# Performance work log

Measured on AMD Instinct MI355X. Metric: run time of the kernel, lower is better.

Reference implementation:

```python
import jax, jax.numpy as jnp
import numpy as np

N_NODES = 100000
N_EDGES = 1600000
D_FEAT = 128
UNITS = 128
LEAKY_ALPHA = 0.2  # tf.nn.leaky_relu default


def setup_inputs() -> dict:
    key = jax.random.key(0)
    k1, k2, k3, k4 = jax.random.split(key, 4)
    node_states = jax.random.normal(k1, (N_NODES, D_FEAT), dtype=jnp.float32)
    edges = jax.random.randint(k2, (N_EDGES, 2), 0, N_NODES, dtype=jnp.int64)
    kernel = jax.random.normal(k3, (D_FEAT, UNITS), dtype=jnp.float32) * (1.0 / np.sqrt(D_FEAT))
    kernel_attention = jax.random.normal(k4, (2 * UNITS, 1), dtype=jnp.float32) * (1.0 / np.sqrt(2 * UNITS))
    return {
        "node_states": node_states,
        "edges": edges,
        "kernel": kernel,
        "kernel_attention": kernel_attention,
    }


def reference(node_states, edges, kernel, kernel_attention):
    n = node_states.shape[0]
    tgt_idx = edges[:, 0]
    src_idx = edges[:, 1]

    # node_states_transformed: [N, units]
    h = node_states @ kernel

    # Attention logits. concat([tgt, src]) @ ka == tgt @ ka_t + src @ ka_s
    # (avoids materializing the [E, 2*units] concat).
    ka_t = kernel_attention[:UNITS, 0]   # [units]
    ka_s = kernel_attention[UNITS:, 0]   # [units]
    score_t = h @ ka_t                   # [N]
    score_s = h @ ka_s                   # [N]
    e = score_t[tgt_idx] + score_s[src_idx]              # [E]
    e = jax.nn.leaky_relu(e, negative_slope=LEAKY_ALPHA)
    e = jnp.exp(jnp.clip(e, -2.0, 2.0))

    # Segment softmax over incoming edges of each target node.
    sum_e = jax.ops.segment_sum(e, tgt_idx, num_segments=n)  # [N]
    attention = e / (sum_e[tgt_idx] + 1e-9)                  # [E]

    # Weighted scatter-sum of source messages.
    messages = h[src_idx] * attention[:, None]               # [E, units]
    output = jax.ops.segment_sum(messages, tgt_idx, num_segments=n)  # [N, units]
    return output
```

## Files before the change

kernel.cpp:

```cpp
#include <hip/hip_runtime.h>
#include <stdint.h>

typedef unsigned short ushort_t;
typedef __attribute__((ext_vector_type(8))) short short8;
typedef __attribute__((ext_vector_type(4))) float float4v;
typedef __attribute__((ext_vector_type(2))) float float2v;

#define N_NODES 100000
#define N_EDGES 1600000
#define D 128
#define NB_GEMM 1563
#define NBP     782
#define NB_B1   250
#define EPB     6400
#define BUCKETS 782
#define CAP     2560

static __device__ __forceinline__ float2v up2(uint32_t u) {
    float2v r;
    r.x = __builtin_bit_cast(float, u << 16);
    r.y = __builtin_bit_cast(float, u & 0xffff0000u);
    return r;
}
static __device__ __forceinline__ ushort_t f2bf(float f) {
    uint32_t u = __builtin_bit_cast(uint32_t, f);
    uint32_t r = u + 0x7fffu + ((u >> 16) & 1u);
    return (ushort_t)(r >> 16);
}
static __device__ __forceinline__ float edge_e(float s) {
    float x = (s >= 0.0f) ? s : 0.2f * s;
    x = fminf(fmaxf(x, -2.0f), 2.0f);
    return __expf(x);
}

__global__ void __launch_bounds__(256) prep_kernel(const float* __restrict__ W,
                                                   const float* __restrict__ KA,
                                                   float* __restrict__ wa,
                                                   ushort_t* __restrict__ WT,
                                                   const int* __restrict__ E,
                                                   int* __restrict__ eflag) {
    __shared__ int s;
    int b = blockIdx.x, t = threadIdx.x;
    int i = b * 256 + t;
    if (b < 64) {
        int k = i >> 7, nn = i & 127;
        int kb = k >> 5, q = (k >> 3) & 3, j = k & 7;
        int tt = nn >> 4, l = nn & 15;
        WT[((kb * 8 + tt) * 64 + q * 16 + l) * 8 + j] = f2bf(W[i]);
    } else if (b == 64) {
        if (t == 0) s = 0;
        __syncthreads();
        int nz = 0;
#pragma unroll
        for (int j = 0; j < 8; j++)
            if (E[(t + j * 256) * 2 + 1] != 0) nz = 1;
        if (nz) atomicOr(&s, 1);
        __syncthreads();
        if (t == 0) *eflag = (s == 0) ? 1 : 0;
    } else if (b == 65) {
        int half = t >> 7, k = t & 127;
        const float* kav = KA + half * 128;
        const float* wrow = W + k * 128;
        float acc = 0.0f;
#pragma unroll 8
        for (int j = 0; j < 128; j++) acc += wrow[j] * kav[j];
        wa[half * 128 + k] = acc;
    }
}

__global__ void __launch_bounds__(256) mega1_kernel(const float* __restrict__ X,
                                                    const ushort_t* __restrict__ WT,
                                                    const float* __restrict__ wa,
                                                    ushort_t* __restrict__ H,
                                                    float* __restrict__ st,
                                                    float* __restrict__ ss,
                                                    int M,
                                                    const int* __restrict__ E,
                                                    const int* __restrict__ eflag,
                                                    int* __restrict__ sortedE,
                                                    ushort_t* __restrict__ bmat,
                                                    ushort_t* __restrict__ lofs) {
    __shared__ ushort_t ob[4][16 * 136];
    if (blockIdx.x >= NBP) {
        int eb = blockIdx.x - NBP;
        int t = threadIdx.x;
        int* lhist = (int*)ob;
        int* lpart = ((int*)ob) + 1024;
        for (int j = t; j < 1024; j += 256) lhist[j] = 0;
        __syncthreads();
        int i64 = *eflag;
        int base = eb * EPB;
        for (int j = 0; j < 25; j++) {
            int i = base + j * 256 + t;
            int tgt = i64 ? E[i * 4] : E[i * 2];
            if ((unsigned)tgt >= (unsigned)N_NODES) tgt = 0;
            atomicAdd(&lhist[tgt >> 7], 1);
        }
        __syncthreads();
        int c0 = lhist[t * 4], c1 = lhist[t * 4 + 1];
        int c2 = lhist[t * 4 + 2], c3 = lhist[t * 4 + 3];
        int sum = c0 + c1 + c2 + c3;
        lpart[t] = sum;
        __syncthreads();
        for (int off = 1; off < 256; off <<= 1) {
            int x = (t >= off) ? lpart[t - off] : 0;
            __syncthreads();
            lpart[t] += x;
            __syncthreads();
        }
        int e0 = lpart[t] - sum;
        int e1 = e0 + c0, e2 = e1 + c1, e3 = e2 + c2;
        int cc[4] = {c0, c1, c2, c3};
        int ee[4] = {e0, e1, e2, e3};
#pragma unroll
        for (int k = 0; k < 4; k++) {
            int bb = t * 4 + k;
            if (bb < BUCKETS) {
                bmat[eb * BUCKETS + bb] = (ushort_t)cc[k];
                lofs[eb * BUCKETS + bb] = (ushort_t)ee[k];
            }
        }
        lhist[t * 4] = e0; lhist[t * 4 + 1] = e1;
        lhist[t * 4 + 2] = e2; lhist[t * 4 + 3] = e3;
        __syncthreads();
        for (int j = 0; j < 25; j++) {
            int i = base + j * 256 + t;
            int tgt, src;
            if (i64) { tgt = E[i * 4]; src = E[i * 4 + 2]; }
            else     { tgt = E[i * 2]; src = E[i * 2 + 1]; }
            if ((unsigned)tgt >= (unsigned)N_NODES) tgt = 0;
            if ((unsigned)src >= (unsigned)N_NODES) src = 0;
            int pos = atomicAdd(&lhist[tgt >> 7], 1);
            if (pos < EPB) sortedE[base + pos] = ((tgt & 127) << 17) | src;
        }
        return;
    }
    int tid = threadIdx.x;
    int wave = tid >> 6, lane = tid & 63;
    int quad = lane >> 4, l16 = lane & 15;
    ushort_t* obw = ob[wave];
    const short8* Bf = (const short8*)WT;

    int t0 = blockIdx.x;
    int nt = (t0 + NBP < NB_GEMM) ? 2 : 1;

    float4 f[8];
    {
        int ar = t0 * 64 + wave * 16 + l16; if (ar >= M) ar = M - 1;
        const float* xr = X + (size_t)ar * D + quad * 8;
#pragma unroll
        for (int kb = 0; kb < 4; kb++) {
            f[kb * 2]     = *(const float4*)(xr + kb * 32);
            f[kb * 2 + 1] = *(const float4*)(xr + kb * 32 + 4);
        }
    }
    for (int it = 0; it < nt; it++) {
        int m0 = (t0 + it * NBP) * 64 + wave * 16;
        float4 nf[8];
        if (it + 1 < nt) {
            int ar = (t0 + NBP) * 64 + wave * 16 + l16; if (ar >= M) ar = M - 1;
            const float* xr = X + (size_t)ar * D + quad * 8;
#pragma unroll
            for (int kb = 0; kb < 4; kb++) {
                nf[kb * 2]     = *(const float4*)(xr + kb * 32);
                nf[kb * 2 + 1] = *(const float4*)(xr + kb * 32 + 4);
            }
        }
        short8 a[4];
        float sct = 0.0f, scs = 0.0f;
#pragma unroll
        for (int kb = 0; kb < 4; kb++) {
            float4 f0 = f[kb * 2], f1 = f[kb * 2 + 1];
            const float* wt0 = wa + kb * 32 + quad * 8;
            float4 t0v = *(const float4*)(wt0);
            float4 t1v = *(const float4*)(wt0 + 4);
            float4 s0v = *(const float4*)(wt0 + 128);
            float4 s1v = *(const float4*)(wt0 + 132);
            sct += f0.x * t0v.x + f0.y * t0v.y + f0.z * t0v.z + f0.w * t0v.w
                 + f1.x * t1v.x + f1.y * t1v.y + f1.z * t1v.z + f1.w * t1v.w;
            scs += f0.x * s0v.x + f0.y * s0v.y + f0.z * s0v.z + f0.w * s0v.w
                 + f1.x * s1v.x + f1.y * s1v.y + f1.z * s1v.z + f1.w * s1v.w;
            short8 v;
            v[0] = (short)f2bf(f0.x); v[1] = (short)f2bf(f0.y);
            v[2] = (short)f2bf(f0.z); v[3] = (short)f2bf(f0.w);
            v[4] = (short)f2bf(f1.x); v[5] = (short)f2bf(f1.y);
            v[6] = (short)f2bf(f1.z); v[7] = (short)f2bf(f1.w);
            a[kb] = v;
        }
        sct += __shfl_xor(sct, 16); sct += __shfl_xor(sct, 32);
        scs += __shfl_xor(scs, 16); scs += __shfl_xor(scs, 32);
        if (quad == 0 && m0 + l16 < M) { st[m0 + l16] = sct; ss[m0 + l16] = scs; }

        float4v acc[8] = {};
#pragma unroll
        for (int kb = 0; kb < 4; kb++) {
#pragma unroll
            for (int t = 0; t < 8; t++) {
                short8 b = Bf[(kb * 8 + t) * 64 + lane];
                acc[t] = __builtin_amdgcn_mfma_f32_16x16x32_bf16(a[kb], b, acc[t], 0, 0, 0);
            }
        }
#pragma unroll
        for (int t = 0; t < 8; t++)
#pragma unroll
            for (int r = 0; r < 4; r++)
                obw[(quad * 4 + r) * 136 + t * 16 + l16] = f2bf(acc[t][r]);
#pragma unroll
        for (int p = 0; p < 4; p++) {
            int row = p * 4 + quad;
            int orow = m0 + row;
            if (orow < M) {
                uint4 v = *(const uint4*)(&obw[row * 136 + l16 * 8]);
                *(uint4*)(H + (size_t)orow * D + l16 * 8) = v;
            }
        }
        if (it + 1 < nt) {
#pragma unroll
            for (int j = 0; j < 8; j++) f[j] = nf[j];
        }
    }
}

__global__ void __launch_bounds__(512) agg2_kernel(const ushort_t* __restrict__ bmat,
                                                   const ushort_t* __restrict__ lofs,
                                                   const int* __restrict__ sortedE,
                                                   const float* __restrict__ st,
                                                   const float* __restrict__ ss,
                                                   const ushort_t* __restrict__ H,
                                                   float* __restrict__ out) {
    __shared__ int stage[CAP];
    __shared__ int sortedLoc[CAP];
    __shared__ int lpart[512];
    __shared__ int lh[128];
    __shared__ int lrp[129];
    int b = blockIdx.x, t = threadIdx.x;
    int cnt = 0, sst = 0;
    if (t < NB_B1) {
        cnt = bmat[t * BUCKETS + b];
        sst = lofs[t * BUCKETS + b];
    }
    lpart[t] = cnt;
    __syncthreads();
    for (int off = 1; off < 512; off <<= 1) {
        int x = (t >= off) ? lpart[t - off] : 0;
        __syncthreads();
        lpart[t] += x;
        __syncthreads();
    }
    int soff  = lpart[t] - cnt;
    int total = lpart[511];
    if (total > CAP) total = CAP;
    if (t < 128) lh[t] = 0;
    for (int k = 0; k < cnt; k++) {
        int idx = soff + k;
        if (idx < CAP) stage[idx] = sortedE[t * EPB + sst + k];
    }
    __syncthreads();
    for (int j = t; j < total; j += 512)
        atomicAdd(&lh[stage[j] >> 17], 1);
    __syncthreads();
    int v = (t < 128) ? lh[t] : 0;
    if (t < 128) lpart[t] = v;
    __syncthreads();
    for (int off = 1; off < 128; off <<= 1) {
        int x = (t >= off && t < 128) ? lpart[t - off] : 0;
        __syncthreads();
        if (t < 128) lpart[t] += x;
        __syncthreads();
    }
    if (t < 128) {
        int ex = lpart[t] - v;
        lrp[t] = ex;
        lh[t]  = ex;
    }
    if (t == 0) lrp[128] = total;
    __syncthreads();
    for (int j = t; j < total; j += 512) {
        int p = stage[j];
        int pos = atomicAdd(&lh[p >> 17], 1);
        if (pos < total) sortedLoc[pos] = p & 0x1FFFF;
    }
    __syncthreads();
    int wave = t >> 6, lane = t & 63;
    int g = lane >> 4, l = lane & 15;
    for (int nd = wave; nd < 128; nd += 8) {
        int gnode = b * 128 + nd;
        if (gnode >= N_NODES) break;
        int start = lrp[nd], end = lrp[nd + 1];
        float stn = st[gnode];
        float den = 0.0f;
        float2v acc2[4] = {};
        int m = start + g;
        for (; m + 4 < end; m += 8) {
            int s0 = sortedLoc[m], s1 = sortedLoc[m + 4];
            float e0 = edge_e(stn + ss[s0]);
            float e1 = edge_e(stn + ss[s1]);
            den += e0 + e1;
            uint4 p0 = *(const uint4*)(H + ((unsigned)s0 << 7) + l * 8);
            uint4 p1 = *(const uint4*)(H + ((unsigned)s1 << 7) + l * 8);
            float2v E0 = {e0, e0}, E1 = {e1, e1};
            acc2[0] += E0 * up2(p0.x) + E1 * up2(p1.x);
            acc2[1] += E0 * up2(p0.y) + E1 * up2(p1.y);
            acc2[2] += E0 * up2(p0.z) + E1 * up2(p1.z);
            acc2[3] += E0 * up2(p0.w) + E1 * up2(p1.w);
        }
        if (m < end) {
            int s0 = sortedLoc[m];
            float e0 = edge_e(stn + ss[s0]);
            den += e0;
            uint4 p0 = *(const uint4*)(H + ((unsigned)s0 << 7) + l * 8);
            float2v E0 = {e0, e0};
            acc2[0] += E0 * up2(p0.x);
            acc2[1] += E0 * up2(p0.y);
            acc2[2] += E0 * up2(p0.z);
            acc2[3] += E0 * up2(p0.w);
        }
        den += __shfl_xor(den, 16);
        den += __shfl_xor(den, 32);
        float r[8];
#pragma unroll
        for (int j = 0; j < 4; j++) {
            float a0 = acc2[j].x, a1 = acc2[j].y;
            a0 += __shfl_xor(a0, 16); a0 += __shfl_xor(a0, 32);
            a1 += __shfl_xor(a1, 16); a1 += __shfl_xor(a1, 32);
            r[j * 2] = a0; r[j * 2 + 1] = a1;
        }
        float inv = 1.0f / (den + 1e-9f);
        if (g == 0) {
            float4 o0 = make_float4(r[0] * inv, r[1] * inv, r[2] * inv, r[3] * inv);
            float4 o1 = make_float4(r[4] * inv, r[5] * inv, r[6] * inv, r[7] * inv);
            *(float4*)(out + (size_t)gnode * D + l * 8) = o0;
            *(float4*)(out + (size_t)gnode * D + l * 8 + 4) = o1;
        }
    }
}

extern "C" void kernel_launch(void* const* d_in, const int* in_sizes, int n_in,
                              void* d_out, int out_size, void* d_ws, size_t ws_size,
                              hipStream_t stream) {
    const float* X  = (const float*)d_in[0];
    const int*   E  = (const int*)d_in[1];
    const float* W  = (const float*)d_in[2];
    const float* KA = (const float*)d_in[3];
    for (int i = 0; i < n_in; i++) {
        int s = in_sizes[i];
        if (s == N_NODES * D)      X  = (const float*)d_in[i];
        else if (s == N_EDGES * 2) E  = (const int*)d_in[i];
        else if (s == D * D)       W  = (const float*)d_in[i];
        else if (s == 2 * D)       KA = (const float*)d_in[i];
    }
    float* out = (float*)d_out;

    char* ws = (char*)d_ws;
    ushort_t* H        = (ushort_t*)(ws + 0);
    float*    wa       = (float*)   (ws + 25600000);
    float*    st       = (float*)   (ws + 25601024);
    float*    ssb      = (float*)   (ws + 26001024);
    int*      sortedE  = (int*)     (ws + 26401024);
    ushort_t* bmat     = (ushort_t*)(ws + 32801024);
    ushort_t* lofs     = (ushort_t*)(ws + 33192032);
    int*      eflag    = (int*)     (ws + 33583040);
    ushort_t* WT       = (ushort_t*)(ws + 33583072);

    prep_kernel<<<66, 256, 0, stream>>>(W, KA, wa, WT, E, eflag);
    mega1_kernel<<<NBP + NB_B1, 256, 0, stream>>>(X, WT, wa, H, st, ssb,
                                                  N_NODES, E, eflag,
                                                  sortedE, bmat, lofs);
    agg2_kernel<<<BUCKETS, 512, 0, stream>>>(bmat, lofs, sortedE, st, ssb,
                                             H, out);
}
```

Before: 229.9 us.

## Store H in permuted column order to drop LDS transpose; shuffle-based scans

The GEMM epilogue now packs each lane's MFMA accumulators straight into bf16 and writes them to H in a permuted column order, removing the LDS staging buffer and its transpose. The aggregation kernel undoes the permutation by writing each lane's eight outputs at stride 16, which replaces two float4 stores with eight scalar stores. The block-level prefix sums in the aggregation kernel switch from barrier-heavy LDS Hillis-Steele loops to wave shuffles plus a small per-wave sum array, which cuts the number of __syncthreads. This trades LDS traffic and barriers for less vectorized output stores.

```diff
diff --git a/kernel.cpp b/kernel.cpp
--- a/kernel.cpp
+++ b/kernel.cpp
@@ -22,10 +22,15 @@
     r.y = __builtin_bit_cast(float, u & 0xffff0000u);
     return r;
 }
+static __device__ __forceinline__ uint32_t f2bf_u(float f) {
+    uint32_t u = __builtin_bit_cast(uint32_t, f);
+    return (u + 0x7fffu + ((u >> 16) & 1u)) >> 16;
+}
 static __device__ __forceinline__ ushort_t f2bf(float f) {
-    uint32_t u = __builtin_bit_cast(uint32_t, f);
-    uint32_t r = u + 0x7fffu + ((u >> 16) & 1u);
-    return (ushort_t)(r >> 16);
+    return (ushort_t)f2bf_u(f);
+}
+static __device__ __forceinline__ uint32_t pack2(float a, float b) {
+    return f2bf_u(a) | (f2bf_u(b) << 16);
 }
 static __device__ __forceinline__ float edge_e(float s) {
     float x = (s >= 0.0f) ? s : 0.2f * s;
@@ -80,12 +85,12 @@
                                                     int* __restrict__ sortedE,
                                                     ushort_t* __restrict__ bmat,
                                                     ushort_t* __restrict__ lofs) {
-    __shared__ ushort_t ob[4][16 * 136];
+    __shared__ int lds_b1[1280];
     if (blockIdx.x >= NBP) {
         int eb = blockIdx.x - NBP;
         int t = threadIdx.x;
-        int* lhist = (int*)ob;
-        int* lpart = ((int*)ob) + 1024;
+        int* lhist = lds_b1;
+        int* lpart = lds_b1 + 1024;
         for (int j = t; j < 1024; j += 256) lhist[j] = 0;
         __syncthreads();
         int i64 = *eflag;
@@ -138,7 +143,6 @@
     int tid = threadIdx.x;
     int wave = tid >> 6, lane = tid & 63;
     int quad = lane >> 4, l16 = lane & 15;
-    ushort_t* obw = ob[wave];
     const short8* Bf = (const short8*)WT;
 
     int t0 = blockIdx.x;
@@ -201,16 +205,14 @@
             }
         }
 #pragma unroll
-        for (int t = 0; t < 8; t++)
-#pragma unroll
-            for (int r = 0; r < 4; r++)
-                obw[(quad * 4 + r) * 136 + t * 16 + l16] = f2bf(acc[t][r]);
-#pragma unroll
-        for (int p = 0; p < 4; p++) {
-            int row = p * 4 + quad;
-            int orow = m0 + row;
+        for (int r = 0; r < 4; r++) {
+            int orow = m0 + quad * 4 + r;
             if (orow < M) {
-                uint4 v = *(const uint4*)(&obw[row * 136 + l16 * 8]);
+                uint4 v;
+                v.x = pack2(acc[0][r], acc[1][r]);
+                v.y = pack2(acc[2][r], acc[3][r]);
+                v.z = pack2(acc[4][r], acc[5][r]);
+                v.w = pack2(acc[6][r], acc[7][r]);
                 *(uint4*)(H + (size_t)orow * D + l16 * 8) = v;
             }
         }
@@ -230,27 +232,34 @@
                                                    float* __restrict__ out) {
     __shared__ int stage[CAP];
     __shared__ int sortedLoc[CAP];
-    __shared__ int lpart[512];
     __shared__ int lh[128];
     __shared__ int lrp[129];
+    __shared__ int wsum[8];
     int b = blockIdx.x, t = threadIdx.x;
+    int lane = t & 63, wv = t >> 6;
     int cnt = 0, sst = 0;
     if (t < NB_B1) {
         cnt = bmat[t * BUCKETS + b];
         sst = lofs[t * BUCKETS + b];
     }
-    lpart[t] = cnt;
-    __syncthreads();
-    for (int off = 1; off < 512; off <<= 1) {
-        int x = (t >= off) ? lpart[t - off] : 0;
-        __syncthreads();
-        lpart[t] += x;
-        __syncthreads();
-    }
-    int soff  = lpart[t] - cnt;
-    int total = lpart[511];
+    int x = cnt;
+#pragma unroll
+    for (int off = 1; off < 64; off <<= 1) {
+        int y = __shfl_up(x, off);
+        if (lane >= off) x += y;
+    }
+    if (lane == 63) wsum[wv] = x;
+    if (t < 128) lh[t] = 0;
+    __syncthreads();
+    int wbase = 0, total = 0;
+#pragma unroll
+    for (int w = 0; w < 8; w++) {
+        int sv = wsum[w];
+        if (w < wv) wbase += sv;
+        total += sv;
+    }
     if (total > CAP) total = CAP;
-    if (t < 128) lh[t] = 0;
+    int soff = wbase + x - cnt;
     for (int k = 0; k < cnt; k++) {
         int idx = soff + k;
         if (idx < CAP) stage[idx] = sortedE[t * EPB + sst + k];
@@ -260,16 +269,17 @@
         atomicAdd(&lh[stage[j] >> 17], 1);
     __syncthreads();
     int v = (t < 128) ? lh[t] : 0;
-    if (t < 128) lpart[t] = v;
-    __syncthreads();
-    for (int off = 1; off < 128; off <<= 1) {
-        int x = (t >= off && t < 128) ? lpart[t - off] : 0;
-        __syncthreads();
-        if (t < 128) lpart[t] += x;
-        __syncthreads();
-    }
+    int xs = v;
+#pragma unroll
+    for (int off = 1; off < 64; off <<= 1) {
+        int y = __shfl_up(xs, off);
+        if (lane >= off) xs += y;
+    }
+    if (t == 63) wsum[0] = xs;
+    __syncthreads();
     if (t < 128) {
-        int ex = lpart[t] - v;
+        int inc = (wv == 1) ? xs + wsum[0] : xs;
+        int ex = inc - v;
         lrp[t] = ex;
         lh[t]  = ex;
     }
@@ -281,9 +291,8 @@
         if (pos < total) sortedLoc[pos] = p & 0x1FFFF;
     }
     __syncthreads();
-    int wave = t >> 6, lane = t & 63;
     int g = lane >> 4, l = lane & 15;
-    for (int nd = wave; nd < 128; nd += 8) {
+    for (int nd = wv; nd < 128; nd += 8) {
         int gnode = b * 128 + nd;
         if (gnode >= N_NODES) break;
         int start = lrp[nd], end = lrp[nd + 1];
@@ -327,10 +336,9 @@
         }
         float inv = 1.0f / (den + 1e-9f);
         if (g == 0) {
-            float4 o0 = make_float4(r[0] * inv, r[1] * inv, r[2] * inv, r[3] * inv);
-            float4 o1 = make_float4(r[4] * inv, r[5] * inv, r[6] * inv, r[7] * inv);
-            *(float4*)(out + (size_t)gnode * D + l * 8) = o0;
-            *(float4*)(out + (size_t)gnode * D + l * 8 + 4) = o1;
+#pragma unroll
+            for (int k = 0; k < 8; k++)
+                out[(size_t)gnode * D + k * 16 + l] = r[k] * inv;
         }
     }
 }
```

Measured after the change: 227.3 us. Within noise of the previous version (-1.1%).
